# Optimization experiments

Measured on AMD Instinct MI355X. Metric: run time of the kernel, lower is better.

## Reference

```python
import jax, jax.numpy as jnp
from jax import lax
import numpy as np

NPOINT, RADIUS, NSAMPLE = 1024, 0.2, 32
MLP, IN_CH, EPS = (64, 64, 128), 6, 1e-5
B, N = 8, 4096


def farthest_point_sample(xyz, npoint):
    # xyz: [B, N, 3] -> idx [B, npoint]. Deterministic start at index 0.
    Bn, Nn, _ = xyz.shape
    def body(carry, _):
        dist, farthest = carry  # dist [B,N], farthest [B]
        centroid = jnp.take_along_axis(xyz, farthest[:, None, None], axis=1)  # [B,1,3]
        d = jnp.sum((xyz - centroid) ** 2, axis=-1)  # [B,N]
        dist = jnp.minimum(dist, d)
        return (dist, jnp.argmax(dist, axis=-1).astype(jnp.int32)), farthest
    init = (jnp.full((Bn, Nn), 1e10, xyz.dtype), jnp.zeros((Bn,), jnp.int32))
    _, idx = lax.scan(body, init, None, length=npoint)  # [npoint, B]
    return idx.T


def query_ball_point(radius, nsample, xyz, new_xyz):
    # xyz [B,N,3], new_xyz [B,S,3] -> idx [B,S,nsample]
    Bn, Nn, _ = xyz.shape
    sq = (jnp.sum(new_xyz ** 2, -1)[:, :, None]
          + jnp.sum(xyz ** 2, -1)[:, None, :]
          - 2.0 * jnp.einsum('bsc,bnc->bsn', new_xyz, xyz))  # [B,S,N]
    gidx = jnp.where(sq > radius ** 2, Nn, jnp.arange(Nn, dtype=jnp.int32)[None, None, :])
    gidx = jnp.sort(gidx, axis=-1)[:, :, :nsample]
    first = gidx[:, :, :1]
    return jnp.where(gidx == Nn, first, gidx)


def setup_inputs():
    key = jax.random.key(0)
    ks = jax.random.split(key, 8)
    inp = {
        'xyz': jax.random.uniform(ks[0], (B, 3, N), dtype=jnp.float32),
        'points': jax.random.normal(ks[1], (B, 3, N), dtype=jnp.float32),
    }
    last = IN_CH
    for i, oc in enumerate(MLP):
        inp[f'w{i}'] = jax.random.normal(ks[2 + i], (oc, last), dtype=jnp.float32) * 0.1
        inp[f'b{i}'] = jnp.zeros((oc,), jnp.float32)
        inp[f'g{i}'] = jnp.ones((oc,), jnp.float32)
        inp[f'be{i}'] = jnp.zeros((oc,), jnp.float32)
        last = oc
    return inp


def reference(xyz, points, w0, b0, g0, be0, w1, b1, g1, be1, w2, b2, g2, be2):
    x = jnp.transpose(xyz, (0, 2, 1))      # [B,N,3]
    p = jnp.transpose(points, (0, 2, 1))   # [B,N,D]
    fidx = farthest_point_sample(x, NPOINT)                       # [B,S]
    new_xyz = jnp.take_along_axis(x, fidx[:, :, None], axis=1)    # [B,S,3]
    idx = query_ball_point(RADIUS, NSAMPLE, x, new_xyz)           # [B,S,K]
    gather = jax.vmap(lambda a, i: a[i])                          # per-batch gather
    grouped_xyz = gather(x, idx)                                  # [B,S,K,3]
    grouped_xyz_norm = grouped_xyz - new_xyz[:, :, None, :]
    grouped_points = gather(p, idx)                               # [B,S,K,D]
    feat = jnp.concatenate([grouped_xyz_norm, grouped_points], axis=-1)  # [B,S,K,C]
    for w, b, g, be in ((w0, b0, g0, be0), (w1, b1, g1, be1), (w2, b2, g2, be2)):
        feat = jnp.einsum('bskc,oc->bsko', feat, w) + b
        mean = feat.mean(axis=(0, 1, 2))
        var = feat.var(axis=(0, 1, 2))
        feat = (feat - mean) * lax.rsqrt(var + EPS) * g + be  # BatchNorm (training stats)
        feat = jax.nn.relu(feat)
    new_points = jnp.max(feat, axis=2)                            # max over K -> [B,S,Cout]
    return jnp.transpose(new_xyz, (0, 2, 1)), jnp.transpose(new_points, (0, 2, 1))
```

## Files before the change

### kernel.cpp

```cpp
#include <hip/hip_runtime.h>
#include <stdint.h>

#define NPTS   4096
#define NPOINT 1024
#define NSAMP  32
#define NROWS  262144
#define RAD2   0.04f

typedef float v2f __attribute__((ext_vector_type(2)));
typedef __attribute__((ext_vector_type(8))) short bf16x8;
typedef __attribute__((ext_vector_type(4))) float f32x4;

__device__ __forceinline__ unsigned short f2bf(float x) {
    unsigned u = __float_as_uint(x);
    return (unsigned short)((u + 0x7FFFu + ((u >> 16) & 1u)) >> 16);
}
__device__ __forceinline__ unsigned pack2bf(float a, float b) {
    return (unsigned)f2bf(a) | ((unsigned)f2bf(b) << 16);
}

#define DPPMAX(v, C)                                                           \
    fmaxf(__int_as_float(__builtin_amdgcn_update_dpp(                          \
              0, __float_as_int(v), C, 0xf, 0xf, true)),                       \
          (v))

__global__ __launch_bounds__(256) void fps_kernel(const float* __restrict__ xyz,
                                                  float* __restrict__ outx)
{
    __shared__ __align__(16) float4 pxyz[NPTS];
    __shared__ __align__(16) float4 orec[NPOINT];
    __shared__ __align__(16) unsigned long long wkey[2][4];
    const int b = blockIdx.x, tid = threadIdx.x;
    const int lane = tid & 63, wid = tid >> 6;
    const float* base = xyz + b * 3 * NPTS;

    float Xs[16], Ys[16], Zs[16];
#pragma unroll
    for (int j = 0; j < 16; ++j) {
        const int n = j * 256 + tid;
        Xs[j] = base[n];
        Ys[j] = base[NPTS + n];
        Zs[j] = base[2 * NPTS + n];
        pxyz[n] = make_float4(Xs[j], Ys[j], Zs[j], 0.0f);
    }
    v2f X2[8], Y2[8], Z2[8], D2[8];
#pragma unroll
    for (int j = 0; j < 8; ++j) {
        X2[j] = (v2f){Xs[2 * j], Xs[2 * j + 1]};
        Y2[j] = (v2f){Ys[2 * j], Ys[2 * j + 1]};
        Z2[j] = (v2f){Zs[2 * j], Zs[2 * j + 1]};
        D2[j] = (v2f){1e10f, 1e10f};
    }
    __syncthreads();
    float4 c4 = pxyz[0];
    float cx = c4.x, cy = c4.y, cz = c4.z;

    for (int t = 0; t < NPOINT; ++t) {
        if (tid == 0) orec[t] = make_float4(cx, cy, cz, 0.0f);
        const v2f cxv = (v2f){cx, cx}, cyv = (v2f){cy, cy}, czv = (v2f){cz, cz};
        float bv = -1.0f; int bi = 0;
#pragma unroll
        for (int j = 0; j < 8; ++j) {
            v2f nd;
            {
#pragma clang fp contract(off)
                const v2f dx = X2[j] - cxv;
                const v2f dy = Y2[j] - cyv;
                const v2f dz = Z2[j] - czv;
                const v2f m0 = dx * dx;
                const v2f m1 = dy * dy;
                const v2f m2 = dz * dz;
                const v2f d = (m0 + m1) + m2;
                nd = __builtin_elementwise_min(D2[j], d);
            }
            D2[j] = nd;
            if (nd.x > bv) { bv = nd.x; bi = j * 512 + tid; }
            if (nd.y > bv) { bv = nd.y; bi = j * 512 + 256 + tid; }
        }
        float rv = bv;
        rv = DPPMAX(rv, 0x111);
        rv = DPPMAX(rv, 0x112);
        rv = DPPMAX(rv, 0x114);
        rv = DPPMAX(rv, 0x118);
        rv = DPPMAX(rv, 0x142);
        rv = DPPMAX(rv, 0x143);
        const unsigned wmax =
            (unsigned)__builtin_amdgcn_readlane(__float_as_int(rv), 63);
        unsigned long long mask = __ballot(__float_as_uint(bv) == wmax);
        unsigned best =
            (unsigned)__builtin_amdgcn_readlane(bi, (int)__builtin_ctzll(mask));
        mask &= mask - 1ull;
        while (mask) {
            const unsigned cand = (unsigned)__builtin_amdgcn_readlane(
                bi, (int)__builtin_ctzll(mask));
            best = cand < best ? cand : best;
            mask &= mask - 1ull;
        }
        if (lane == 0)
            wkey[t & 1][wid] = ((unsigned long long)wmax << 32) |
                               (unsigned)(~best);
        __syncthreads();
        const ulonglong2* wk = (const ulonglong2*)wkey[t & 1];
        const ulonglong2 ka = wk[0], kb = wk[1];
        unsigned long long kk = ka.x;
        if (ka.y > kk) kk = ka.y;
        if (kb.x > kk) kk = kb.x;
        if (kb.y > kk) kk = kb.y;
        const int farthest = (int)(~(unsigned)kk) & (NPTS - 1);
        c4 = pxyz[farthest];
        cx = c4.x; cy = c4.y; cz = c4.z;
    }
    __syncthreads();
    float* ox = outx + b * 3 * NPOINT;
    for (int i = tid; i < NPOINT; i += 256) {
        const float4 c = orec[i];
        ox[i]              = c.x;
        ox[NPOINT + i]     = c.y;
        ox[2 * NPOINT + i] = c.z;
    }
}

__global__ __launch_bounds__(256) void ball_kernel(const float* __restrict__ xyz,
                                                   const float* __restrict__ pts,
                                                   const float* __restrict__ outx,
                                                   int* __restrict__ idxbuf,
                                                   float* __restrict__ mom,
                                                   uint4* __restrict__ featbuf)
{
    __shared__ float red[4][42];
    const int tid = threadIdx.x;
    const int w = blockIdx.x * 4 + (tid >> 6);
    const int lane = tid & 63, wid = tid >> 6;
    const int b = w >> 10, s = w & 1023;
    const float* base = xyz + b * 3 * NPTS;
    const float cx = outx[b * 3 * NPOINT + s];
    const float cy = outx[b * 3 * NPOINT + NPOINT + s];
    const float cz = outx[b * 3 * NPOINT + 2 * NPOINT + s];
    const float sumS = __fadd_rn(__fadd_rn(__fmul_rn(cx, cx), __fmul_rn(cy, cy)),
                                 __fmul_rn(cz, cz));
    int cnt = 0, first_n = -1;
    int* myidx = idxbuf + w * NSAMP;

    for (int chunk = 0; chunk < NPTS / 64 && cnt < NSAMP; ++chunk) {
        const int n = chunk * 64 + lane;
        float nx = base[n], ny = base[NPTS + n], nz = base[2 * NPTS + n];
        float sumN = __fadd_rn(__fadd_rn(__fmul_rn(nx, nx), __fmul_rn(ny, ny)),
                               __fmul_rn(nz, nz));
        float dot = __fadd_rn(__fadd_rn(__fmul_rn(cx, nx), __fmul_rn(cy, ny)),
                              __fmul_rn(cz, nz));
        float sq = __fsub_rn(__fadd_rn(sumS, sumN), __fmul_rn(2.0f, dot));
        bool keep = (sq <= RAD2);
        unsigned long long mask = __ballot(keep);
        if (first_n < 0 && mask) first_n = chunk * 64 + (int)__builtin_ctzll(mask);
        int pos = cnt + __popcll(mask & ((1ull << lane) - 1ull));
        if (keep && pos < NSAMP) myidx[pos] = n;
        cnt += __popcll(mask);
    }
    if (cnt < NSAMP) {
        if (lane >= cnt && lane < NSAMP) myidx[lane] = first_n;
    }

    float m[42];
#pragma unroll
    for (int i = 0; i < 42; ++i) m[i] = 0.f;
    if (lane < 32) {
        const int idx = myidx[lane];
        const float* pb = pts + b * 3 * NPTS;
        float f[6];
        f[0] = base[idx] - cx;
        f[1] = base[NPTS + idx] - cy;
        f[2] = base[2 * NPTS + idx] - cz;
        f[3] = pb[idx];
        f[4] = pb[NPTS + idx];
        f[5] = pb[2 * NPTS + idx];
        featbuf[w * NSAMP + lane] =
            make_uint4(pack2bf(f[0], f[1]), pack2bf(f[2], f[3]),
                       pack2bf(f[4], f[5]), 0u);
#pragma unroll
        for (int c = 0; c < 6; ++c) m[c] = f[c];
#pragma unroll
        for (int c = 0; c < 6; ++c)
#pragma unroll
            for (int d = 0; d < 6; ++d)
                m[6 + c * 6 + d] = f[c] * f[d];
    }
#pragma unroll
    for (int i = 0; i < 42; ++i) {
        float v = m[i];
        v += __shfl_xor(v, 1);  v += __shfl_xor(v, 2);  v += __shfl_xor(v, 4);
        v += __shfl_xor(v, 8);  v += __shfl_xor(v, 16); v += __shfl_xor(v, 32);
        m[i] = v;
    }
    if (lane == 0) {
#pragma unroll
        for (int i = 0; i < 42; ++i) red[wid][i] = m[i];
    }
    __syncthreads();
    if (tid < 42)
        atomicAdd(&mom[tid], red[0][tid] + red[1][tid] + red[2][tid] + red[3][tid]);
}

__device__ __forceinline__ void compute_bn0(int o, const float* __restrict__ mom,
                                            const float* __restrict__ w0,
                                            const float* __restrict__ g,
                                            const float* __restrict__ be,
                                            float* __restrict__ sbn0)
{
    float w[6];
#pragma unroll
    for (int c = 0; c < 6; ++c) w[c] = w0[o * 6 + c];
    const float inv = 1.0f / (float)NROWS;
    float mean = 0.f;
#pragma unroll
    for (int c = 0; c < 6; ++c) mean = fmaf(w[c], mom[c], mean);
    mean *= inv;
    float ey2 = 0.f;
#pragma unroll
    for (int c = 0; c < 6; ++c) {
        float t = 0.f;
#pragma unroll
        for (int d = 0; d < 6; ++d) t = fmaf(w[d], mom[6 + c * 6 + d], t);
        ey2 = fmaf(w[c], t, ey2);
    }
    ey2 *= inv;
    const float var = ey2 - mean * mean;
    const float scale = g[o] * rsqrtf(var + 1e-5f);
    sbn0[o] = scale;
    sbn0[64 + o] = be[o] - mean * scale;
}

#define XP  72
#define WP  72
#define W0P 40

__global__ __launch_bounds__(256, 2) void mlp1_kernel(
    const uint4* __restrict__ featbuf,
    const float* __restrict__ w0, const float* __restrict__ mom,
    const float* __restrict__ g0, const float* __restrict__ be0,
    const float* __restrict__ w1, float* __restrict__ stats)
{
    __shared__ __align__(16) unsigned short sw0[64 * W0P];
    __shared__ __align__(16) unsigned short sw1[64 * WP];
    __shared__ __align__(16) unsigned short xb[4][32 * XP];
    __shared__ float sbn0[128];
    __shared__ float red[4][128];
    const int tid = threadIdx.x, lane = tid & 63, wid = tid >> 6;

    for (int i = tid; i < 64 * W0P / 2; i += 256) ((unsigned*)sw0)[i] = 0;
    if (tid < 64) compute_bn0(tid, mom, w0, g0, be0, sbn0);
    __syncthreads();
    for (int i = tid; i < 192; i += 256) {
        const int o = i / 3, c = (i % 3) * 2;
        *(unsigned*)&sw0[o * W0P + c] = pack2bf(w0[o * 6 + c], w0[o * 6 + c + 1]);
    }
    for (int i = tid; i < 2048; i += 256) {
        const int o = i >> 5, k = (i & 31) * 2;
        *(unsigned*)&sw1[o * WP + k] = pack2bf(w1[o * 64 + k], w1[o * 64 + k + 1]);
    }

    const int mh = lane & 15, q = lane >> 4;
    unsigned short* X = xb[wid];
    const int rbase = blockIdx.x * 512 + wid * 32;
    float sA[4] = {0.f, 0.f, 0.f, 0.f}, qA[4] = {0.f, 0.f, 0.f, 0.f};

    for (int c = 0; c < 4; ++c) {
        __syncthreads();
        if (lane < 32) {
            const int r = rbase + c * 128 + lane;
            uint4* xq = (uint4*)&xb[wid][lane * XP];
            xq[0] = featbuf[r];
            xq[1] = make_uint4(0u, 0u, 0u, 0u);
            xq[2] = make_uint4(0u, 0u, 0u, 0u);
            xq[3] = make_uint4(0u, 0u, 0u, 0u);
        }
        __syncthreads();
        f32x4 acc0[2][4] = {};
        {
            bf16x8 a[2], bw[4];
#pragma unroll
            for (int mt = 0; mt < 2; ++mt)
                a[mt] = *(const bf16x8*)&X[(mt * 16 + mh) * XP + q * 8];
#pragma unroll
            for (int nt = 0; nt < 4; ++nt)
                bw[nt] = *(const bf16x8*)&sw0[(nt * 16 + mh) * W0P + q * 8];
#pragma unroll
            for (int mt = 0; mt < 2; ++mt)
#pragma unroll
                for (int nt = 0; nt < 4; ++nt)
                    acc0[mt][nt] = __builtin_amdgcn_mfma_f32_16x16x32_bf16(
                        a[mt], bw[nt], acc0[mt][nt], 0, 0, 0);
        }
        __syncthreads();
#pragma unroll
        for (int nt = 0; nt < 4; ++nt) {
            const int ch = nt * 16 + mh;
            const float sc = sbn0[ch], sh = sbn0[64 + ch];
#pragma unroll
            for (int mt = 0; mt < 2; ++mt)
#pragma unroll
                for (int rr = 0; rr < 4; ++rr) {
                    const float v = fmaxf(fmaf(acc0[mt][nt][rr], sc, sh), 0.0f);
                    X[(mt * 16 + q * 4 + rr) * XP + ch] = f2bf(v);
                }
        }
        __syncthreads();
        f32x4 acc1[2][4] = {};
#pragma unroll
        for (int ks = 0; ks < 2; ++ks) {
            bf16x8 a[2], bw[4];
#pragma unroll
            for (int mt = 0; mt < 2; ++mt)
                a[mt] = *(const bf16x8*)&X[(mt * 16 + mh) * XP + ks * 32 + q * 8];
#pragma unroll
            for (int nt = 0; nt < 4; ++nt)
                bw[nt] = *(const bf16x8*)&sw1[(nt * 16 + mh) * WP + ks * 32 + q * 8];
#pragma unroll
            for (int mt = 0; mt < 2; ++mt)
#pragma unroll
                for (int nt = 0; nt < 4; ++nt)
                    acc1[mt][nt] = __builtin_amdgcn_mfma_f32_16x16x32_bf16(
                        a[mt], bw[nt], acc1[mt][nt], 0, 0, 0);
        }
#pragma unroll
        for (int nt = 0; nt < 4; ++nt)
#pragma unroll
            for (int mt = 0; mt < 2; ++mt)
#pragma unroll
                for (int rr = 0; rr < 4; ++rr) {
                    const float v = acc1[mt][nt][rr];
                    sA[nt] += v;
                    qA[nt] = fmaf(v, v, qA[nt]);
                }
    }
#pragma unroll
    for (int nt = 0; nt < 4; ++nt) {
        float s = sA[nt], qq = qA[nt];
        s += __shfl_xor(s, 16); qq += __shfl_xor(qq, 16);
        s += __shfl_xor(s, 32); qq += __shfl_xor(qq, 32);
        if (q == 0) {
            red[wid][nt * 16 + mh] = s;
            red[wid][64 + nt * 16 + mh] = qq;
        }
    }
    __syncthreads();
    if (tid < 128)
        atomicAdd(&stats[tid],
                  red[0][tid] + red[1][tid] + red[2][tid] + red[3][tid]);
}

__global__ __launch_bounds__(256, 2) void mlp2_kernel(
    const uint4* __restrict__ featbuf,
    const float* __restrict__ w0, const float* __restrict__ mom,
    const float* __restrict__ g0, const float* __restrict__ be0,
    const float* __restrict__ w1, const float* __restrict__ stats1,
    const float* __restrict__ g1, const float* __restrict__ be1,
    const float* __restrict__ w2,
    float* __restrict__ stats, float* __restrict__ gmax)
{
    __shared__ __align__(16) unsigned short sw0[64 * W0P];
    __shared__ __align__(16) unsigned short sw1[64 * WP];
    __shared__ __align__(16) unsigned short sw2[128 * WP];
    __shared__ __align__(16) unsigned short xb[4][32 * XP];
    __shared__ float sbn0[128];
    __shared__ float sbn1[128];
    __shared__ float red[4][256];
    const int tid = threadIdx.x, lane = tid & 63, wid = tid >> 6;

    for (int i = tid; i < 64 * W0P / 2; i += 256) ((unsigned*)sw0)[i] = 0;
    if (tid < 64) {
        compute_bn0(tid, mom, w0, g0, be0, sbn0);
    } else if (tid < 128) {
        const int ch = tid - 64;
        const float inv = 1.0f / (float)NROWS;
        const float mean = stats1[ch] * inv;
        const float var = stats1[64 + ch] * inv - mean * mean;
        const float scale = g1[ch] * rsqrtf(var + 1e-5f);
        sbn1[ch] = scale;
        sbn1[64 + ch] = be1[ch] - mean * scale;
    }
    __syncthreads();
    for (int i = tid; i < 192; i += 256) {
        const int o = i / 3, c = (i % 3) * 2;
        *(unsigned*)&sw0[o * W0P + c] = pack2bf(w0[o * 6 + c], w0[o * 6 + c + 1]);
    }
    for (int i = tid; i < 2048; i += 256) {
        const int o = i >> 5, k = (i & 31) * 2;
        *(unsigned*)&sw1[o * WP + k] = pack2bf(w1[o * 64 + k], w1[o * 64 + k + 1]);
    }
    for (int i = tid; i < 4096; i += 256) {
        const int o = i >> 5, k = (i & 31) * 2;
        *(unsigned*)&sw2[o * WP + k] = pack2bf(w2[o * 64 + k], w2[o * 64 + k + 1]);
    }

    const int mh = lane & 15, q = lane >> 4;
    unsigned short* X = xb[wid];
    const int rbase = blockIdx.x * 512 + wid * 32;
    float sA[8], qA[8];
#pragma unroll
    for (int i = 0; i < 8; ++i) { sA[i] = 0.f; qA[i] = 0.f; }

    for (int c = 0; c < 4; ++c) {
        __syncthreads();
        if (lane < 32) {
            const int r = rbase + c * 128 + lane;
            uint4* xq = (uint4*)&xb[wid][lane * XP];
            xq[0] = featbuf[r];
            xq[1] = make_uint4(0u, 0u, 0u, 0u);
            xq[2] = make_uint4(0u, 0u, 0u, 0u);
            xq[3] = make_uint4(0u, 0u, 0u, 0u);
        }
        __syncthreads();
        f32x4 acc0[2][4] = {};
        {
            bf16x8 a[2], bw[4];
#pragma unroll
            for (int mt = 0; mt < 2; ++mt)
                a[mt] = *(const bf16x8*)&X[(mt * 16 + mh) * XP + q * 8];
#pragma unroll
            for (int nt = 0; nt < 4; ++nt)
                bw[nt] = *(const bf16x8*)&sw0[(nt * 16 + mh) * W0P + q * 8];
#pragma unroll
            for (int mt = 0; mt < 2; ++mt)
#pragma unroll
                for (int nt = 0; nt < 4; ++nt)
                    acc0[mt][nt] = __builtin_amdgcn_mfma_f32_16x16x32_bf16(
                        a[mt], bw[nt], acc0[mt][nt], 0, 0, 0);
        }
        __syncthreads();
#pragma unroll
        for (int nt = 0; nt < 4; ++nt) {
            const int ch = nt * 16 + mh;
            const float sc = sbn0[ch], sh = sbn0[64 + ch];
#pragma unroll
            for (int mt = 0; mt < 2; ++mt)
#pragma unroll
                for (int rr = 0; rr < 4; ++rr) {
                    const float v = fmaxf(fmaf(acc0[mt][nt][rr], sc, sh), 0.0f);
                    X[(mt * 16 + q * 4 + rr) * XP + ch] = f2bf(v);
                }
        }
        __syncthreads();
        f32x4 acc1[2][4] = {};
#pragma unroll
        for (int ks = 0; ks < 2; ++ks) {
            bf16x8 a[2], bw[4];
#pragma unroll
            for (int mt = 0; mt < 2; ++mt)
                a[mt] = *(const bf16x8*)&X[(mt * 16 + mh) * XP + ks * 32 + q * 8];
#pragma unroll
            for (int nt = 0; nt < 4; ++nt)
                bw[nt] = *(const bf16x8*)&sw1[(nt * 16 + mh) * WP + ks * 32 + q * 8];
#pragma unroll
            for (int mt = 0; mt < 2; ++mt)
#pragma unroll
                for (int nt = 0; nt < 4; ++nt)
                    acc1[mt][nt] = __builtin_amdgcn_mfma_f32_16x16x32_bf16(
                        a[mt], bw[nt], acc1[mt][nt], 0, 0, 0);
        }
        __syncthreads();
#pragma unroll
        for (int nt = 0; nt < 4; ++nt) {
            const int ch = nt * 16 + mh;
            const float sc = sbn1[ch], sh = sbn1[64 + ch];
#pragma unroll
            for (int mt = 0; mt < 2; ++mt)
#pragma unroll
                for (int rr = 0; rr < 4; ++rr) {
                    const float v = fmaxf(fmaf(acc1[mt][nt][rr], sc, sh), 0.0f);
                    X[(mt * 16 + q * 4 + rr) * XP + ch] = f2bf(v);
                }
        }
        __syncthreads();
        const int g = blockIdx.x * 16 + c * 4 + wid;
        bf16x8 a2[2][2];
#pragma unroll
        for (int mt = 0; mt < 2; ++mt)
#pragma unroll
            for (int ks = 0; ks < 2; ++ks)
                a2[mt][ks] = *(const bf16x8*)&X[(mt * 16 + mh) * XP + ks * 32 + q * 8];
#pragma unroll
        for (int nt = 0; nt < 8; ++nt) {
            f32x4 acc[2] = {};
#pragma unroll
            for (int ks = 0; ks < 2; ++ks) {
                const bf16x8 bw = *(const bf16x8*)&sw2[(nt * 16 + mh) * WP + ks * 32 + q * 8];
#pragma unroll
                for (int mt = 0; mt < 2; ++mt)
                    acc[mt] = __builtin_amdgcn_mfma_f32_16x16x32_bf16(
                        a2[mt][ks], bw, acc[mt], 0, 0, 0);
            }
            float m = -3.0e38f;
#pragma unroll
            for (int mt = 0; mt < 2; ++mt)
#pragma unroll
                for (int rr = 0; rr < 4; ++rr) {
                    const float v = acc[mt][rr];
                    sA[nt] += v;
                    qA[nt] = fmaf(v, v, qA[nt]);
                    m = fmaxf(m, v);
                }
            m = fmaxf(m, __shfl_xor(m, 16));
            m = fmaxf(m, __shfl_xor(m, 32));
            if (q == 0) gmax[(nt * 16 + mh) * 8192 + g] = m;
        }
    }
#pragma unroll
    for (int nt = 0; nt < 8; ++nt) {
        float s = sA[nt], qq = qA[nt];
        s += __shfl_xor(s, 16); qq += __shfl_xor(qq, 16);
        s += __shfl_xor(s, 32); qq += __shfl_xor(qq, 32);
        if (q == 0) {
            red[wid][nt * 16 + mh] = s;
            red[wid][128 + nt * 16 + mh] = qq;
        }
    }
    __syncthreads();
    atomicAdd(&stats[tid],
              red[0][tid] + red[1][tid] + red[2][tid] + red[3][tid]);
}

__global__ __launch_bounds__(256) void final_kernel(const float* __restrict__ gmax,
                                                    const float* __restrict__ stats2,
                                                    const float* __restrict__ g2,
                                                    const float* __restrict__ be2,
                                                    float* __restrict__ out2)
{
    __shared__ float sbn[256];
    const int tid = threadIdx.x;
    if (tid < 128) {
        const float inv = 1.0f / (float)NROWS;
        const float mean = stats2[tid] * inv;
        const float var = stats2[128 + tid] * inv - mean * mean;
        const float scale = g2[tid] * rsqrtf(var + 1e-5f);
        sbn[tid] = scale;
        sbn[128 + tid] = be2[tid] - mean * scale;
    }
    __syncthreads();
    const int t = blockIdx.x * 256 + tid;
    const int s = t & 1023;
    const int o = (t >> 10) & 127;
    const int b = t >> 17;
    const int g = (b << 10) | s;
    float v = gmax[o * 8192 + g];
    v = fmaf(v, sbn[o], sbn[128 + o]);
    out2[t] = fmaxf(v, 0.0f);
}

extern "C" void kernel_launch(void* const* d_in, const int* in_sizes, int n_in,
                              void* d_out, int out_size, void* d_ws, size_t ws_size,
                              hipStream_t stream)
{
    const float* xyz = (const float*)d_in[0];
    const float* pts = (const float*)d_in[1];
    const float* w0  = (const float*)d_in[2];
    const float* g0  = (const float*)d_in[4];
    const float* be0 = (const float*)d_in[5];
    const float* w1  = (const float*)d_in[6];
    const float* g1  = (const float*)d_in[8];
    const float* be1 = (const float*)d_in[9];
    const float* w2  = (const float*)d_in[10];
    const float* g2  = (const float*)d_in[12];
    const float* be2 = (const float*)d_in[13];

    float* out_xyz = (float*)d_out;
    float* out2    = out_xyz + 8 * 3 * NPOINT;

    char* wsb = (char*)d_ws;
    int*   idxbuf  = (int*)(wsb + 32768);
    float* stats   = (float*)(wsb + 32768 + 1048576);
    float* gmax    = stats + 1024;
    uint4* featbuf = (uint4*)(gmax + 128 * 8192);

    float* mom    = stats;
    float* stats1 = stats + 128;
    float* stats2 = stats + 256;

    hipMemsetAsync(stats, 0, 512 * sizeof(float), stream);

    fps_kernel<<<8, 256, 0, stream>>>(xyz, out_xyz);
    ball_kernel<<<2048, 256, 0, stream>>>(xyz, pts, out_xyz, idxbuf, mom, featbuf);
    mlp1_kernel<<<512, 256, 0, stream>>>(featbuf, w0, mom, g0, be0, w1, stats1);
    mlp2_kernel<<<512, 256, 0, stream>>>(featbuf, w0, mom, g0, be0,
                                         w1, stats1, g1, be1,
                                         w2, stats2, gmax);
    final_kernel<<<4096, 256, 0, stream>>>(gmax, stats2, g2, be2, out2);
}
```

Before: 798.5 us.

## Store layer-1 activations in bf16 and skip recomputing layers 0-1 in mlp2

When the workspace is large enough, mlp1 now writes its pre-BN layer-1 outputs as bf16 to a buffer. A new mlp2b kernel reads that buffer, applies BN1 and ReLU, and runs only the layer-2 GEMM, so layers 0 and 1 are no longer recomputed. The ball kernel also keeps its neighbor indices in shared memory instead of a global buffer. In exchange, each layer-1 tile is stored twice, once as the bf16 activations and once implicitly through the stats, which costs extra global writes and reads. Whether the new path runs depends on the workspace size.

```diff
diff --git a/kernel.cpp b/kernel.cpp
--- a/kernel.cpp
+++ b/kernel.cpp
@@ -123,11 +123,11 @@
 __global__ __launch_bounds__(256) void ball_kernel(const float* __restrict__ xyz,
                                                    const float* __restrict__ pts,
                                                    const float* __restrict__ outx,
-                                                   int* __restrict__ idxbuf,
                                                    float* __restrict__ mom,
                                                    uint4* __restrict__ featbuf)
 {
     __shared__ float red[4][42];
+    __shared__ int smyidx[4][NSAMP];
     const int tid = threadIdx.x;
     const int w = blockIdx.x * 4 + (tid >> 6);
     const int lane = tid & 63, wid = tid >> 6;
@@ -139,7 +139,7 @@
     const float sumS = __fadd_rn(__fadd_rn(__fmul_rn(cx, cx), __fmul_rn(cy, cy)),
                                  __fmul_rn(cz, cz));
     int cnt = 0, first_n = -1;
-    int* myidx = idxbuf + w * NSAMP;
+    int* myidx = smyidx[wid];
 
     for (int chunk = 0; chunk < NPTS / 64 && cnt < NSAMP; ++chunk) {
         const int n = chunk * 64 + lane;
@@ -237,7 +237,8 @@
     const uint4* __restrict__ featbuf,
     const float* __restrict__ w0, const float* __restrict__ mom,
     const float* __restrict__ g0, const float* __restrict__ be0,
-    const float* __restrict__ w1, float* __restrict__ stats)
+    const float* __restrict__ w1, float* __restrict__ stats,
+    uint4* __restrict__ l1store)
 {
     __shared__ __align__(16) unsigned short sw0[64 * W0P];
     __shared__ __align__(16) unsigned short sw1[64 * WP];
@@ -331,6 +332,26 @@
                     sA[nt] += v;
                     qA[nt] = fmaf(v, v, qA[nt]);
                 }
+        if (l1store) {
+#pragma unroll
+            for (int nt = 0; nt < 4; ++nt) {
+                const int ch = nt * 16 + mh;
+#pragma unroll
+                for (int mt = 0; mt < 2; ++mt)
+#pragma unroll
+                    for (int rr = 0; rr < 4; ++rr)
+                        X[(mt * 16 + q * 4 + rr) * XP + ch] =
+                            f2bf(acc1[mt][nt][rr]);
+            }
+            uint4* dst = l1store +
+                         (size_t)(blockIdx.x * 16 + c * 4 + wid) * 256;
+#pragma unroll
+            for (int k = 0; k < 4; ++k) {
+                const int idx = lane * 4 + k;
+                const int row = idx >> 3, c8 = (idx & 7) * 8;
+                dst[idx] = *(const uint4*)&X[row * XP + c8];
+            }
+        }
     }
 #pragma unroll
     for (int nt = 0; nt < 4; ++nt) {
@@ -346,6 +367,116 @@
     if (tid < 128)
         atomicAdd(&stats[tid],
                   red[0][tid] + red[1][tid] + red[2][tid] + red[3][tid]);
+}
+
+__global__ __launch_bounds__(256, 2) void mlp2b_kernel(
+    const uint4* __restrict__ l1buf,
+    const float* __restrict__ stats1,
+    const float* __restrict__ g1, const float* __restrict__ be1,
+    const float* __restrict__ w2,
+    float* __restrict__ stats, float* __restrict__ gmax)
+{
+    __shared__ __align__(16) unsigned short sw2[128 * WP];
+    __shared__ float sbn1[128];
+    __shared__ float red[4][256];
+    const int tid = threadIdx.x, lane = tid & 63, wid = tid >> 6;
+
+    if (tid < 64) {
+        const float inv = 1.0f / (float)NROWS;
+        const float mean = stats1[tid] * inv;
+        const float var = stats1[64 + tid] * inv - mean * mean;
+        const float scale = g1[tid] * rsqrtf(var + 1e-5f);
+        sbn1[tid] = scale;
+        sbn1[64 + tid] = be1[tid] - mean * scale;
+    }
+    for (int i = tid; i < 4096; i += 256) {
+        const int o = i >> 5, k = (i & 31) * 2;
+        *(unsigned*)&sw2[o * WP + k] = pack2bf(w2[o * 64 + k], w2[o * 64 + k + 1]);
+    }
+    __syncthreads();
+
+    const int mh = lane & 15, q = lane >> 4;
+    float sc[2][8], sh[2][8];
+#pragma unroll
+    for (int ks = 0; ks < 2; ++ks)
+#pragma unroll
+        for (int j = 0; j < 8; ++j) {
+            const int ch = ks * 32 + q * 8 + j;
+            sc[ks][j] = sbn1[ch];
+            sh[ks][j] = sbn1[64 + ch];
+        }
+
+    float sA[8], qA[8];
+#pragma unroll
+    for (int i = 0; i < 8; ++i) { sA[i] = 0.f; qA[i] = 0.f; }
+
+    for (int c = 0; c < 4; ++c) {
+        const int g = blockIdx.x * 16 + c * 4 + wid;
+        const uint4* src = l1buf + (size_t)g * 256;
+        bf16x8 a2[2][2];
+#pragma unroll
+        for (int mt = 0; mt < 2; ++mt)
+#pragma unroll
+            for (int ks = 0; ks < 2; ++ks) {
+                const int row = mt * 16 + mh;
+                const uint4 v = src[row * 8 + ks * 4 + q];
+                const unsigned* pv = (const unsigned*)&v;
+                unsigned r[4];
+#pragma unroll
+                for (int p = 0; p < 4; ++p) {
+                    const unsigned u = pv[p];
+                    const float f0 = __uint_as_float(u << 16);
+                    const float f1 = __uint_as_float(u & 0xFFFF0000u);
+                    const float v0 =
+                        fmaxf(fmaf(f0, sc[ks][2 * p], sh[ks][2 * p]), 0.0f);
+                    const float v1 =
+                        fmaxf(fmaf(f1, sc[ks][2 * p + 1], sh[ks][2 * p + 1]),
+                              0.0f);
+                    r[p] = pack2bf(v0, v1);
+                }
+                const uint4 packed = make_uint4(r[0], r[1], r[2], r[3]);
+                a2[mt][ks] = __builtin_bit_cast(bf16x8, packed);
+            }
+#pragma unroll
+        for (int nt = 0; nt < 8; ++nt) {
+            f32x4 acc[2] = {};
+#pragma unroll
+            for (int ks = 0; ks < 2; ++ks) {
+                const bf16x8 bw =
+                    *(const bf16x8*)&sw2[(nt * 16 + mh) * WP + ks * 32 + q * 8];
+#pragma unroll
+                for (int mt = 0; mt < 2; ++mt)
+                    acc[mt] = __builtin_amdgcn_mfma_f32_16x16x32_bf16(
+                        a2[mt][ks], bw, acc[mt], 0, 0, 0);
+            }
+            float m = -3.0e38f;
+#pragma unroll
+            for (int mt = 0; mt < 2; ++mt)
+#pragma unroll
+                for (int rr = 0; rr < 4; ++rr) {
+                    const float v = acc[mt][rr];
+                    sA[nt] += v;
+                    qA[nt] = fmaf(v, v, qA[nt]);
+                    m = fmaxf(m, v);
+                }
+            m = fmaxf(m, __shfl_xor(m, 16));
+            m = fmaxf(m, __shfl_xor(m, 32));
+            if (q == 0) gmax[(nt * 16 + mh) * 8192 + g] = m;
+        }
+    }
+#pragma unroll
+    for (int nt = 0; nt < 8; ++nt) {
+        float s = sA[nt], qq = qA[nt];
+        s += __shfl_xor(s, 16); qq += __shfl_xor(qq, 16);
+        s += __shfl_xor(s, 32); qq += __shfl_xor(qq, 32);
+        if (q == 0) {
+            red[wid][nt * 16 + mh] = s;
+            red[wid][128 + nt * 16 + mh] = qq;
+        }
+    }
+    __syncthreads();
+    atomicAdd(&stats[tid],
+              red[0][tid] + red[1][tid] + red[2][tid] + red[3][tid]);
 }
 
 __global__ __launch_bounds__(256, 2) void mlp2_kernel(
@@ -566,22 +697,32 @@
     float* out2    = out_xyz + 8 * 3 * NPOINT;
 
     char* wsb = (char*)d_ws;
-    int*   idxbuf  = (int*)(wsb + 32768);
     float* stats   = (float*)(wsb + 32768 + 1048576);
     float* gmax    = stats + 1024;
     uint4* featbuf = (uint4*)(gmax + 128 * 8192);
+    uint4* l1buf   = featbuf + NROWS;
 
     float* mom    = stats;
     float* stats1 = stats + 128;
     float* stats2 = stats + 256;
 
+    const bool bigws = ws_size >= (size_t)43100000;
+
     hipMemsetAsync(stats, 0, 512 * sizeof(float), stream);
 
     fps_kernel<<<8, 256, 0, stream>>>(xyz, out_xyz);
-    ball_kernel<<<2048, 256, 0, stream>>>(xyz, pts, out_xyz, idxbuf, mom, featbuf);
-    mlp1_kernel<<<512, 256, 0, stream>>>(featbuf, w0, mom, g0, be0, w1, stats1);
-    mlp2_kernel<<<512, 256, 0, stream>>>(featbuf, w0, mom, g0, be0,
-                                         w1, stats1, g1, be1,
-                                         w2, stats2, gmax);
+    ball_kernel<<<2048, 256, 0, stream>>>(xyz, pts, out_xyz, mom, featbuf);
+    if (bigws) {
+        mlp1_kernel<<<512, 256, 0, stream>>>(featbuf, w0, mom, g0, be0,
+                                             w1, stats1, l1buf);
+        mlp2b_kernel<<<512, 256, 0, stream>>>(l1buf, stats1, g1, be1,
+                                              w2, stats2, gmax);
+    } else {
+        mlp1_kernel<<<512, 256, 0, stream>>>(featbuf, w0, mom, g0, be0,
+                                             w1, stats1, nullptr);
+        mlp2_kernel<<<512, 256, 0, stream>>>(featbuf, w0, mom, g0, be0,
+                                             w1, stats1, g1, be1,
+                                             w2, stats2, gmax);
+    }
     final_kernel<<<4096, 256, 0, stream>>>(gmax, stats2, g2, be2, out2);
 }
```

Result: no change. 793.3 us (-0.7%).
